# Kernel tuning notes

Measured on AMD Instinct MI355X. Metric: run time of the kernel, lower is better.

Reference implementation:

```python
import jax, jax.numpy as jnp
import numpy as np

N = 50000      # nodes
DEG = 32       # avg degree
E = N * DEG + N  # edges incl. self loops
IN_DIM = 512
H = 4          # heads
D = 128        # hidden per head
SLOPE = 0.2


def setup_inputs() -> dict:
    key = jax.random.key(0)
    ks = jax.random.split(key, 12)
    features = jax.random.normal(ks[0], (N, IN_DIM), dtype=jnp.float32)
    src_r = jax.random.randint(ks[1], (N * DEG,), 0, N)
    dst_r = jax.random.randint(ks[2], (N * DEG,), 0, N)
    loop = jnp.arange(N)
    src = jnp.concatenate([src_r, loop]).astype(jnp.int32)
    dst = jnp.concatenate([dst_r, loop]).astype(jnp.int32)
    ids = jax.random.randint(ks[3], (16,), 0, N)
    s0 = 1.0 / np.sqrt(IN_DIM)
    s1 = 1.0 / np.sqrt(H * D)
    fc_w0 = jax.random.normal(ks[4], (IN_DIM, H * D), dtype=jnp.float32) * s0
    attn_l0 = jax.random.normal(ks[5], (H, D), dtype=jnp.float32) * s1
    attn_r0 = jax.random.normal(ks[6], (H, D), dtype=jnp.float32) * s1
    bias0 = jnp.zeros((H * D,), dtype=jnp.float32)
    fc_w1 = jax.random.normal(ks[7], (H * D, H * D), dtype=jnp.float32) * s1
    attn_l1 = jax.random.normal(ks[8], (H, D), dtype=jnp.float32) * s1
    attn_r1 = jax.random.normal(ks[9], (H, D), dtype=jnp.float32) * s1
    bias1 = jnp.zeros((H * D,), dtype=jnp.float32)
    return dict(features=features, fc_w0=fc_w0, attn_l0=attn_l0, attn_r0=attn_r0,
                bias0=bias0, fc_w1=fc_w1, attn_l1=attn_l1, attn_r1=attn_r1,
                bias1=bias1, src=src, dst=dst, ids=ids)


def gat_layer(h, fc_w, attn_l, attn_r, bias, src, dst, residual):
    ft = (h @ fc_w).reshape(N, H, D)                     # [N,H,D]
    el = jnp.sum(ft * attn_l, axis=-1)                   # [N,H]
    er = jnp.sum(ft * attn_r, axis=-1)                   # [N,H]
    e = jax.nn.leaky_relu(el[src] + er[dst], SLOPE)      # [E,H]
    # edge softmax over incoming edges of each dst node (self-loops guarantee coverage)
    emax = jax.ops.segment_max(e, dst, num_segments=N)   # [N,H]
    ee = jnp.exp(e - emax[dst])
    esum = jax.ops.segment_sum(ee, dst, num_segments=N)  # [N,H]
    alpha = ee / esum[dst]                               # [E,H]
    out = jax.ops.segment_sum(alpha[:, :, None] * ft[src], dst, num_segments=N)  # [N,H,D]
    if residual:
        out = out + h.reshape(N, H, D)                   # res_fc is Identity (in == H*D)
    out = out + bias.reshape(1, H, D)
    out = jax.nn.elu(out)
    return out.reshape(N, H * D)


def reference(features, fc_w0, attn_l0, attn_r0, bias0, fc_w1, attn_l1, attn_r1,
              bias1, src, dst, ids):
    h = gat_layer(features, fc_w0, attn_l0, attn_r0, bias0, src, dst, residual=False)
    h = gat_layer(h, fc_w1, attn_l1, attn_r1, bias1, src, dst, residual=True)
    h = jnp.tanh(h)
    return h[ids]  # [B, H*D] gather per id2node lookup
```

## Files before the change

### kernel.cpp

```cpp
#include <hip/hip_runtime.h>
#include <hip/hip_bf16.h>

typedef short bf16x8 __attribute__((ext_vector_type(8)));
typedef float f32x4 __attribute__((ext_vector_type(4)));

#define HD 512
#define KDIM 512
#define NHEAD 4
#define DHEAD 128
#define C1CAP 1024
#define C2CAP 16384
#define E1CAP 2048
#define E2CAP 32768

struct PassSM {
    unsigned bm[1568];
    int2 eBuf[256];
    int fBuf[256];
    int sid[16];
    int eCnt, fCnt, eBase, fBase, s_c;
};

union PrepSM {
    PassSM pass;
    float tile[64][65];
    int s_c;
};

struct GemmSM {
    __hip_bfloat16 As[128][40];
    __hip_bfloat16 Bs[128][40];
    float pel[2][128];
    float perr[2][128];
};

__device__ int detect_bf16(const unsigned short* f, int* s_c) {
    int c = 0;
#pragma unroll
    for (int k = 0; k < 4; ++k) {
        unsigned short u = f[2 * (threadIdx.x + k * 256)];
        int e = (u >> 7) & 0xFF;
        c += (e >= 96 && e <= 140) ? 1 : 0;
    }
#pragma unroll
    for (int off = 32; off; off >>= 1) c += __shfl_xor(c, off, 64);
    if (threadIdx.x == 0) *s_c = 0;
    __syncthreads();
    if ((threadIdx.x & 63) == 0) atomicAdd(s_c, c);
    __syncthreads();
    int r = (*s_c > 512) ? 1 : 0;
    __syncthreads();
    return r;
}

template<int MODE>
__device__ void pass_scan(int pid, const int* __restrict__ src,
                          const int* __restrict__ dst, int E, int B,
                          const int* __restrict__ map1g, PassSM& sm,
                          int2* __restrict__ elist, int* ecnt, int ecap,
                          int* __restrict__ cntArr,
                          int* __restrict__ mapm, int* __restrict__ Flist,
                          int* nFr, int fcap) {
    const int t = threadIdx.x;
    const int nq = E >> 2;
    const int gid = pid * 256 + t;
    if (gid < nq) {
        const int4 d4 = ((const int4*)dst)[gid];
        const int dv[4] = {d4.x, d4.y, d4.z, d4.w};
#pragma unroll
        for (int k = 0; k < 4; ++k) {
            const int d = dv[k];
            if ((sm.bm[d >> 5] >> (d & 31)) & 1u) {
                const int e = 4 * gid + k;
                int slot;
                if (MODE == 0) {
                    slot = 0;
                    for (int q = 0; q < B; ++q) if (sm.sid[q] == d) slot = q;
                } else {
                    slot = map1g[d]; if (slot < 0) slot = 0;
                }
                int p = atomicAdd(&cntArr[slot], 1);
                int2 v; v.x = src[e]; v.y = slot | (p << (MODE == 0 ? 4 : 10));
                int pp = atomicAdd(&sm.eCnt, 1);
                if (pp < 256) sm.eBuf[pp] = v;
                else { int q = atomicAdd(ecnt, 1); if (q < ecap) elist[q] = v; }
                const int s = v.x;
                if (atomicCAS(&mapm[s], -1, -2) == -1) {
                    int q = atomicAdd(&sm.fCnt, 1);
                    if (q < 256) sm.fBuf[q] = s;
                    else {
                        int g2 = atomicAdd(nFr, 1);
                        if (g2 < fcap) { Flist[g2] = s; mapm[s] = g2; }
                        else mapm[s] = 0;
                    }
                }
            }
        }
    }
    __syncthreads();
    const int ne = (sm.eCnt < 256) ? sm.eCnt : 256;
    const int nf = (sm.fCnt < 256) ? sm.fCnt : 256;
    if (t == 0 && ne) sm.eBase = atomicAdd(ecnt, ne);
    if (t == 64 && nf) sm.fBase = atomicAdd(nFr, nf);
    __syncthreads();
    for (int i = t; i < ne; i += 256) {
        int pos = sm.eBase + i;
        if (pos < ecap) elist[pos] = sm.eBuf[i];
    }
    for (int i = t; i < nf; i += 256) {
        int q = sm.fBase + i; int s = sm.fBuf[i];
        if (q < fcap) { Flist[q] = s; mapm[s] = q; }
        else mapm[s] = 0;
    }
}

__device__ void gemm_tile(const __hip_bfloat16* __restrict__ A,
                          const __hip_bfloat16* __restrict__ Bt,
                          __hip_bfloat16* __restrict__ C,
                          const float* __restrict__ al_, const float* __restrict__ ar_,
                          float* __restrict__ el, float* __restrict__ er,
                          int cntv, int m0, int n0, GemmSM& sm) {
    const int t = threadIdx.x;
    const int lane = t & 63, wave = t >> 6;
    const int wm = (wave >> 1) * 64, wn = (wave & 1) * 64;
    const int fr = lane & 15, fk = (lane >> 4) * 8;
    const int r0 = t >> 2;
    const int c0 = (t & 3) * 8;

    int arow[2];
#pragma unroll
    for (int r = 0; r < 2; ++r) {
        int rr = m0 + r * 64 + r0;
        if (rr >= cntv) rr = cntv - 1;
        arow[r] = rr;
    }

    auto loadAB = [&](int kt, uint4 va[2], uint4 vb[2]) {
#pragma unroll
        for (int r = 0; r < 2; ++r) {
            va[r] = *(const uint4*)&A[(size_t)arow[r] * KDIM + kt + c0];
            int row = r * 64 + r0;
            vb[r] = *(const uint4*)&Bt[(size_t)(n0 + row) * KDIM + kt + c0];
        }
    };

    f32x4 acc[4][4];
#pragma unroll
    for (int i = 0; i < 4; ++i)
#pragma unroll
        for (int j = 0; j < 4; ++j)
#pragma unroll
            for (int r = 0; r < 4; ++r) acc[i][j][r] = 0.f;

    uint4 cva[2], cvb[2], nva[2], nvb[2];
    loadAB(0, cva, cvb);
    for (int kt = 0; kt < KDIM; kt += 32) {
#pragma unroll
        for (int r = 0; r < 2; ++r) {
            int row = r * 64 + r0;
            *(uint4*)&sm.As[row][c0] = cva[r];
            *(uint4*)&sm.Bs[row][c0] = cvb[r];
        }
        __syncthreads();
        if (kt + 32 < KDIM) loadAB(kt + 32, nva, nvb);
        bf16x8 af[4], bfr[4];
#pragma unroll
        for (int i = 0; i < 4; ++i) af[i]  = *(const bf16x8*)&sm.As[wm + i * 16 + fr][fk];
#pragma unroll
        for (int j = 0; j < 4; ++j) bfr[j] = *(const bf16x8*)&sm.Bs[wn + j * 16 + fr][fk];
#pragma unroll
        for (int i = 0; i < 4; ++i)
#pragma unroll
            for (int j = 0; j < 4; ++j)
                acc[i][j] = __builtin_amdgcn_mfma_f32_16x16x32_bf16(af[i], bfr[j], acc[i][j], 0, 0, 0);
        __syncthreads();
#pragma unroll
        for (int r = 0; r < 2; ++r) { cva[r] = nva[r]; cvb[r] = nvb[r]; }
    }

    const int cr = (lane >> 4) * 4;
    const int cc = lane & 15;
#pragma unroll
    for (int i = 0; i < 4; ++i)
#pragma unroll
        for (int j = 0; j < 4; ++j)
#pragma unroll
            for (int rg = 0; rg < 4; ++rg) {
                int m = m0 + wm + i * 16 + cr + rg;
                int n = n0 + wn + j * 16 + cc;
                C[(size_t)m * HD + n] = __float2bfloat16(acc[i][j][rg]);
            }

    const int h = n0 >> 7;
    float alv[4], arv[4];
#pragma unroll
    for (int j = 0; j < 4; ++j) {
        alv[j] = al_[h * DHEAD + wn + j * 16 + cc];
        arv[j] = ar_[h * DHEAD + wn + j * 16 + cc];
    }
#pragma unroll
    for (int i = 0; i < 4; ++i)
#pragma unroll
        for (int rg = 0; rg < 4; ++rg) {
            float sl = 0.f, sr = 0.f;
#pragma unroll
            for (int j = 0; j < 4; ++j) {
                float c = acc[i][j][rg];
                sl += c * alv[j];
                sr += c * arv[j];
            }
#pragma unroll
            for (int off = 1; off < 16; off <<= 1) {
                sl += __shfl_xor(sl, off, 16);
                sr += __shfl_xor(sr, off, 16);
            }
            if (cc == 0) {
                int row = wm + i * 16 + cr + rg;
                sm.pel[wn >> 6][row] = sl;
                sm.perr[wn >> 6][row] = sr;
            }
        }
    __syncthreads();
    if (t < 128) {
        int m = m0 + t;
        if (m < cntv) {
            el[m * NHEAD + h] = sm.pel[0][t] + sm.pel[1][t];
            er[m * NHEAD + h] = sm.perr[0][t] + sm.perr[1][t];
        }
    }
    __syncthreads();
}

__global__ __launch_bounds__(256) void prep_pass1_k(
    const void* __restrict__ features,
    const void* __restrict__ W0, const void* __restrict__ W1,
    __hip_bfloat16* __restrict__ Wt0, __hip_bfloat16* __restrict__ Wt1,
    const void* p0, const void* p1, const void* p2,
    const void* p3, const void* p4, const void* p5,
    float* __restrict__ smallc,
    const int* __restrict__ ids, int B, int* __restrict__ mapId,
    const int* __restrict__ src, const int* __restrict__ dst, int E,
    int2* __restrict__ E1l, int* __restrict__ counters,
    int* __restrict__ cnt1, int* __restrict__ map1, int* __restrict__ F1list) {
    __shared__ PrepSM sm;
    const int b = blockIdx.x;
    const int t = threadIdx.x;
    if (b < 128) {
        const int isbf = detect_bf16((const unsigned short*)features, &sm.s_c);
        const int mtx = b >> 6;
        const int tidx = b & 63;
        const int i0 = (tidx >> 3) * 64, j0 = (tidx & 7) * 64;
        const void* W = mtx ? W1 : W0;
        __hip_bfloat16* Wt = mtx ? Wt1 : Wt0;
        const int rr = t >> 6, cc = t & 63;
#pragma unroll
        for (int it = 0; it < 16; ++it) {
            int ii = rr + it * 4;
            size_t idx = (size_t)(i0 + ii) * 512 + j0 + cc;
            float v = isbf ? __bfloat162float(((const __hip_bfloat16*)W)[idx])
                           : ((const float*)W)[idx];
            sm.tile[ii][cc] = v;
        }
        __syncthreads();
#pragma unroll
        for (int it = 0; it < 16; ++it) {
            int jj = rr + it * 4;
            Wt[(size_t)(j0 + jj) * 512 + i0 + cc] = __float2bfloat16(sm.tile[cc][jj]);
        }
    } else if (b < 134) {
        const int isbf = detect_bf16((const unsigned short*)features, &sm.s_c);
        int which = b - 128;
        const void* p;
        switch (which) {
            case 0: p = p0; break;
            case 1: p = p1; break;
            case 2: p = p2; break;
            case 3: p = p3; break;
            case 4: p = p4; break;
            default: p = p5; break;
        }
#pragma unroll
        for (int r = 0; r < 2; ++r) {
            int e = t + r * 256;
            float v = isbf ? __bfloat162float(((const __hip_bfloat16*)p)[e])
                           : ((const float*)p)[e];
            smallc[which * 512 + e] = v;
        }
    } else if (b == 134) {
        if (t < B) atomicMax(&mapId[ids[t]], t);
    } else {
        const int pid = b - 135;
        for (int i = t; i < 1568; i += 256) sm.pass.bm[i] = 0u;
        if (t < 16) sm.pass.sid[t] = (t < B) ? ids[t] : -1;
        if (t == 0) { sm.pass.eCnt = 0; sm.pass.fCnt = 0; }
        __syncthreads();
        if (t < B) { int n = sm.pass.sid[t]; atomicOr(&sm.pass.bm[n >> 5], 1u << (n & 31)); }
        __syncthreads();
        pass_scan<0>(pid, src, dst, E, B, nullptr, sm.pass,
                     E1l, counters + 0, E1CAP, cnt1,
                     map1, F1list, counters + 2, C1CAP);
    }
}

__global__ __launch_bounds__(256) void pass2_k(
    const int* __restrict__ src, const int* __restrict__ dst, int E,
    const int* __restrict__ F1list, int* __restrict__ counters,
    const int* __restrict__ map1,
    int2* __restrict__ E2l, int* __restrict__ cnt2,
    int* __restrict__ map2, int* __restrict__ F2list) {
    __shared__ PassSM sm;
    const int t = threadIdx.x;
    for (int i = t; i < 1568; i += 256) sm.bm[i] = 0u;
    if (t == 0) { sm.eCnt = 0; sm.fCnt = 0; }
    __syncthreads();
    int nf1 = counters[2]; if (nf1 > C1CAP) nf1 = C1CAP;
    for (int i = t; i < nf1; i += 256) {
        int n = F1list[i];
        atomicOr(&sm.bm[n >> 5], 1u << (n & 31));
    }
    __syncthreads();
    pass_scan<1>(blockIdx.x, src, dst, E, 0, map1, sm,
                 E2l, counters + 1, E2CAP, cnt2,
                 map2, F2list, counters + 3, C2CAP);
}

__global__ __launch_bounds__(256) void gather_k(
    const void* __restrict__ feat, const int* __restrict__ F2list,
    const int* __restrict__ nF2p, __hip_bfloat16* __restrict__ Ac) {
    __shared__ int s_c;
    const int isbf = detect_bf16((const unsigned short*)feat, &s_c);
    int cnt = *nF2p; if (cnt > C2CAP) cnt = C2CAP;
    const int t = threadIdx.x;
    for (int b = blockIdx.x; b < cnt; b += gridDim.x) {
        int row = F2list[b];
        __hip_bfloat162 v;
        if (isbf) {
            v = *(const __hip_bfloat162*)&((const __hip_bfloat16*)feat)[(size_t)row * KDIM + t * 2];
        } else {
            const float2 f = *(const float2*)&((const float*)feat)[(size_t)row * KDIM + t * 2];
            v.x = __float2bfloat16(f.x);
            v.y = __float2bfloat16(f.y);
        }
        *(__hip_bfloat162*)&Ac[(size_t)b * KDIM + t * 2] = v;
    }
}

__global__ __launch_bounds__(256) void gemmel_k(
    int do_scatter,
    const int2* __restrict__ E1l, const int2* __restrict__ E2l,
    const int* __restrict__ counters,
    const int* __restrict__ cnt1, const int* __restrict__ cnt2,
    const int* __restrict__ map1, const int* __restrict__ map2,
    int* __restrict__ off1, int* __restrict__ off2,
    int* __restrict__ b1, int* __restrict__ b2,
    const __hip_bfloat16* __restrict__ A,
    const __hip_bfloat16* __restrict__ Bt, __hip_bfloat16* __restrict__ C,
    const float* __restrict__ al_, const float* __restrict__ ar_,
    float* __restrict__ el, float* __restrict__ er,
    const int* __restrict__ countp, int cap) {
    __shared__ alignas(16) GemmSM sm;
    const int t = threadIdx.x;
    const int bid = blockIdx.x;
    if (do_scatter && bid == 0) {
        int* soff = (int*)&sm;
        int* sc   = soff + 1024;
        int* s1   = sc + 256;
        int c0 = cnt2[t * 4 + 0], c1 = cnt2[t * 4 + 1];
        int c2 = cnt2[t * 4 + 2], c3 = cnt2[t * 4 + 3];
        int tsum = c0 + c1 + c2 + c3;
        sc[t] = tsum;
        __syncthreads();
        for (int off = 1; off < 256; off <<= 1) {
            int x = (t >= off) ? sc[t - off] : 0;
            __syncthreads();
            sc[t] += x;
            __syncthreads();
        }
        int run = sc[t] - tsum;
        int b4 = t * 4;
        off2[b4 + 0] = run; soff[b4 + 0] = run; run += c0;
        off2[b4 + 1] = run; soff[b4 + 1] = run; run += c1;
        off2[b4 + 2] = run; soff[b4 + 2] = run; run += c2;
        off2[b4 + 3] = run; soff[b4 + 3] = run; run += c3;
        if (t == 255) off2[1024] = run;
        if (t == 0) {
            int acc = 0;
            for (int i = 0; i < 16; ++i) { off1[i] = acc; s1[i] = acc; acc += cnt1[i]; }
            off1[16] = acc;
        }
        __syncthreads();
        int n2 = counters[1]; if (n2 > E2CAP) n2 = E2CAP;
        for (int i = t; i < n2; i += 256) {
            int2 v = E2l[i];
            int y = v.y & 1023, p = v.y >> 10;
            int pos = soff[y] + p;
            int r = map2[v.x]; if (r < 0) r = 0;
            if (pos < E2CAP) b2[pos] = r;
        }
        int n1 = counters[0]; if (n1 > E1CAP) n1 = E1CAP;
        for (int i = t; i < n1; i += 256) {
            int2 v = E1l[i];
            int y = v.y & 15, p = v.y >> 4;
            int pos = s1[y] + p;
            int r = map1[v.x]; if (r < 0) r = 0;
            if (pos < E1CAP) b1[pos] = r;
        }
        return;
    }
    const int nblk = (int)gridDim.x - (do_scatter ? 1 : 0);
    const int start = bid - (do_scatter ? 1 : 0);
    int cntv = *countp; if (cntv > cap) cntv = cap;
    const int nt = ((cntv + 127) >> 7) * 4;
    for (int tile = start; tile < nt; tile += nblk)
        gemm_tile(A, Bt, C, al_, ar_, el, er,
                  cntv, (tile >> 2) * 128, (tile & 3) * 128, sm);
}

__global__ __launch_bounds__(256) void agg1_k(
    const int* __restrict__ off2, const int* __restrict__ b2,
    const int* __restrict__ F1list, const int* __restrict__ map2,
    const int* __restrict__ nF1p,
    const float* __restrict__ el, const float* __restrict__ er,
    const __hip_bfloat16* __restrict__ ftc,
    const float* __restrict__ bias,
    __hip_bfloat16* __restrict__ outc) {
    int b = blockIdx.x;
    if (b >= *nF1p) return;
    int n = F1list[b];
    const int h = threadIdx.x >> 6, lane = threadIdx.x & 63;
    int rn = map2[n]; if (rn < 0) rn = 0;
    float ern = er[rn * NHEAD + h];
    int beg = off2[b], end = off2[b + 1];
    float m = -3.0e38f, l = 0.f, a0 = 0.f, a1 = 0.f;
    int i = beg;
    for (; i + 4 <= end; i += 4) {
        int r4[4]; float ev[4]; __hip_bfloat162 fv[4];
#pragma unroll
        for (int k = 0; k < 4; ++k) {
            int r = b2[i + k]; if ((unsigned)r >= C2CAP) r = 0;
            r4[k] = r;
        }
#pragma unroll
        for (int k = 0; k < 4; ++k) {
            ev[k] = el[r4[k] * NHEAD + h];
            fv[k] = *(const __hip_bfloat162*)&ftc[(size_t)r4[k] * HD + h * DHEAD + lane * 2];
        }
#pragma unroll
        for (int k = 0; k < 4; ++k) {
            float e = ev[k] + ern;
            e = (e >= 0.f) ? e : 0.2f * e;
            float mn = fmaxf(m, e);
            float sc = __expf(m - mn);
            float w  = __expf(e - mn);
            l  = l * sc + w;
            a0 = a0 * sc + w * __bfloat162float(fv[k].x);
            a1 = a1 * sc + w * __bfloat162float(fv[k].y);
            m = mn;
        }
    }
    for (; i < end; ++i) {
        int r2 = b2[i]; if ((unsigned)r2 >= C2CAP) r2 = 0;
        float e = el[r2 * NHEAD + h] + ern;
        e = (e >= 0.f) ? e : 0.2f * e;
        float mn = fmaxf(m, e);
        float sc = __expf(m - mn);
        float w  = __expf(e - mn);
        const __hip_bfloat162 f = *(const __hip_bfloat162*)&ftc[(size_t)r2 * HD + h * DHEAD + lane * 2];
        l  = l * sc + w;
        a0 = a0 * sc + w * __bfloat162float(f.x);
        a1 = a1 * sc + w * __bfloat162float(f.y);
        m = mn;
    }
    float inv = (l > 0.f) ? 1.0f / l : 0.f;
    float o0 = a0 * inv, o1 = a1 * inv;
    const float2 bb = *(const float2*)&bias[h * DHEAD + lane * 2];
    o0 += bb.x; o1 += bb.y;
    o0 = (o0 > 0.f) ? o0 : expm1f(o0);
    o1 = (o1 > 0.f) ? o1 : expm1f(o1);
    __hip_bfloat162 o2;
    o2.x = __float2bfloat16(o0);
    o2.y = __float2bfloat16(o1);
    *(__hip_bfloat162*)&outc[(size_t)b * HD + h * DHEAD + lane * 2] = o2;
}

__global__ __launch_bounds__(256) void agg2_k(
    const int* __restrict__ off1, const int* __restrict__ b1,
    const int* __restrict__ ids, const int* __restrict__ mapId,
    const int* __restrict__ map1,
    const float* __restrict__ el, const float* __restrict__ er,
    const __hip_bfloat16* __restrict__ ftc,
    const __hip_bfloat16* __restrict__ resc,
    const float* __restrict__ bias,
    void* __restrict__ out, const void* __restrict__ features) {
    __shared__ int s_c;
    const int isbf = detect_bf16((const unsigned short*)features, &s_c);
    int b = blockIdx.x;
    int n = ids[b];
    int slot = mapId[n]; if (slot < 0) slot = 0;
    const int h = threadIdx.x >> 6, lane = threadIdx.x & 63;
    int rn = map1[n]; if (rn < 0) rn = 0;
    float ern = er[rn * NHEAD + h];
    int beg = off1[slot], end = off1[slot + 1];
    float m = -3.0e38f, l = 0.f, a0 = 0.f, a1 = 0.f;
    int i = beg;
    for (; i + 4 <= end; i += 4) {
        int r4[4]; float ev[4]; __hip_bfloat162 fv[4];
#pragma unroll
        for (int k = 0; k < 4; ++k) {
            int r = b1[i + k]; if ((unsigned)r >= C1CAP) r = 0;
            r4[k] = r;
        }
#pragma unroll
        for (int k = 0; k < 4; ++k) {
            ev[k] = el[r4[k] * NHEAD + h];
            fv[k] = *(const __hip_bfloat162*)&ftc[(size_t)r4[k] * HD + h * DHEAD + lane * 2];
        }
#pragma unroll
        for (int k = 0; k < 4; ++k) {
            float e = ev[k] + ern;
            e = (e >= 0.f) ? e : 0.2f * e;
            float mn = fmaxf(m, e);
            float sc = __expf(m - mn);
            float w  = __expf(e - mn);
            l  = l * sc + w;
            a0 = a0 * sc + w * __bfloat162float(fv[k].x);
            a1 = a1 * sc + w * __bfloat162float(fv[k].y);
            m = mn;
        }
    }
    for (; i < end; ++i) {
        int r1 = b1[i]; if ((unsigned)r1 >= C1CAP) r1 = 0;
        float e = el[r1 * NHEAD + h] + ern;
        e = (e >= 0.f) ? e : 0.2f * e;
        float mn = fmaxf(m, e);
        float sc = __expf(m - mn);
        float w  = __expf(e - mn);
        const __hip_bfloat162 f = *(const __hip_bfloat162*)&ftc[(size_t)r1 * HD + h * DHEAD + lane * 2];
        l  = l * sc + w;
        a0 = a0 * sc + w * __bfloat162float(f.x);
        a1 = a1 * sc + w * __bfloat162float(f.y);
        m = mn;
    }
    float inv = (l > 0.f) ? 1.0f / l : 0.f;
    float o0 = a0 * inv, o1 = a1 * inv;
    const __hip_bfloat162 rv = *(const __hip_bfloat162*)&resc[(size_t)rn * HD + h * DHEAD + lane * 2];
    o0 += __bfloat162float(rv.x);
    o1 += __bfloat162float(rv.y);
    const float2 bb = *(const float2*)&bias[h * DHEAD + lane * 2];
    o0 += bb.x; o1 += bb.y;
    o0 = (o0 > 0.f) ? o0 : expm1f(o0);
    o1 = (o1 > 0.f) ? o1 : expm1f(o1);
    o0 = tanhf(o0);
    o1 = tanhf(o1);
    size_t oi = (size_t)b * HD + h * DHEAD + lane * 2;
    if (isbf) {
        __hip_bfloat162 o2;
        o2.x = __float2bfloat16(o0);
        o2.y = __float2bfloat16(o1);
        *(__hip_bfloat162*)&((__hip_bfloat16*)out)[oi] = o2;
    } else {
        float2 o2; o2.x = o0; o2.y = o1;
        *(float2*)&((float*)out)[oi] = o2;
    }
}

extern "C" void kernel_launch(void* const* d_in, const int* in_sizes, int n_in,
                              void* d_out, int out_size, void* d_ws, size_t ws_size,
                              hipStream_t stream) {
    const void* features = d_in[0];
    const int* src = (const int*)d_in[9];
    const int* dst = (const int*)d_in[10];
    const int* ids = (const int*)d_in[11];

    const int N = in_sizes[0] / KDIM;
    const int E = in_sizes[9];
    const int B = in_sizes[11];

    char* w = (char*)d_ws;
    auto alloc = [&](size_t bytes) {
        void* p = (void*)w;
        w += (bytes + 255) & ~(size_t)255;
        return p;
    };
    __hip_bfloat16* Wt0 = (__hip_bfloat16*)alloc(512 * 512 * 2);
    __hip_bfloat16* Wt1 = (__hip_bfloat16*)alloc(512 * 512 * 2);
    float* smallc = (float*)alloc(6 * 512 * 4);
    int* maps  = (int*)alloc((size_t)3 * N * 4);
    int* mapId = maps;
    int* map1  = maps + N;
    int* map2  = maps + 2 * N;
    int2* E1l  = (int2*)alloc((size_t)E1CAP * 8);
    int2* E2l  = (int2*)alloc((size_t)E2CAP * 8);
    int* F1list = (int*)alloc(C1CAP * 4);
    int* F2list = (int*)alloc(C2CAP * 4);
    const int zwords = 8 + 16 + 1024;
    int* zmem = (int*)alloc((size_t)zwords * 4);
    int* counters = zmem;
    int* cnt1 = zmem + 8;
    int* cnt2 = cnt1 + 16;
    int* off1 = (int*)alloc(17 * 4);
    int* off2 = (int*)alloc(1025 * 4);
    int* b1   = (int*)alloc(E1CAP * 4);
    int* b2   = (int*)alloc(E2CAP * 4);
    __hip_bfloat16* Ac   = (__hip_bfloat16*)alloc((size_t)C2CAP * KDIM * 2);
    __hip_bfloat16* ft0c = (__hip_bfloat16*)alloc((size_t)C2CAP * HD * 2);
    float* el0 = (float*)alloc((size_t)C2CAP * NHEAD * 4);
    float* er0 = (float*)alloc((size_t)C2CAP * NHEAD * 4);
    __hip_bfloat16* h1c  = (__hip_bfloat16*)alloc((size_t)C1CAP * HD * 2);
    __hip_bfloat16* ft1c = (__hip_bfloat16*)alloc((size_t)C1CAP * HD * 2);
    float* el1 = (float*)alloc((size_t)C1CAP * NHEAD * 4);
    float* er1 = (float*)alloc((size_t)C1CAP * NHEAD * 4);

    hipMemsetAsync(maps, 0xFF, (size_t)3 * N * 4, stream);
    hipMemsetAsync(zmem, 0, (size_t)zwords * 4, stream);

    float* al0c = smallc + 0 * 512;
    float* ar0c = smallc + 1 * 512;
    float* b0c  = smallc + 2 * 512;
    float* al1c = smallc + 3 * 512;
    float* ar1c = smallc + 4 * 512;
    float* b1c  = smallc + 5 * 512;

    const int nblk_scan = (E / 4 + 255) / 256;

    prep_pass1_k<<<135 + nblk_scan, 256, 0, stream>>>(
        features, d_in[1], d_in[5], Wt0, Wt1,
        d_in[2], d_in[3], d_in[4], d_in[6], d_in[7], d_in[8],
        smallc, ids, B, mapId, src, dst, E,
        E1l, counters, cnt1, map1, F1list);

    pass2_k<<<nblk_scan, 256, 0, stream>>>(src, dst, E, F1list, counters, map1,
                                           E2l, cnt2, map2, F2list);

    gather_k<<<2048, 256, 0, stream>>>(features, F2list, counters + 3, Ac);

    gemmel_k<<<513, 256, 0, stream>>>(1, E1l, E2l, counters, cnt1, cnt2,
                                      map1, map2, off1, off2, b1, b2,
                                      Ac, Wt0, ft0c, al0c, ar0c, el0, er0,
                                      counters + 3, C2CAP);

    agg1_k<<<C1CAP, 256, 0, stream>>>(off2, b2, F1list, map2, counters + 2,
                                      el0, er0, ft0c, b0c, h1c);

    gemmel_k<<<32, 256, 0, stream>>>(0, E1l, E2l, counters, cnt1, cnt2,
                                     map1, map2, off1, off2, b1, b2,
                                     h1c, Wt1, ft1c, al1c, ar1c, el1, er1,
                                     counters + 2, C1CAP);

    agg2_k<<<B, 256, 0, stream>>>(off1, b1, ids, mapId, map1,
                                  el1, er1, ft1c, h1c, b1c,
                                  d_out, features);
}
```

Baseline: 362.8 us.

## Move edge scatter into gather kernel and spread it across blocks

```diff
diff --git a/kernel.cpp b/kernel.cpp
--- a/kernel.cpp
+++ b/kernel.cpp
@@ -12,6 +12,7 @@
 #define C2CAP 16384
 #define E1CAP 2048
 #define E2CAP 32768
+#define SCATB 64
 
 struct PassSM {
     unsigned bm[1568];
@@ -324,47 +325,22 @@
                  map2, F2list, counters + 3, C2CAP);
 }
 
-__global__ __launch_bounds__(256) void gather_k(
+__global__ __launch_bounds__(256) void gathscat_k(
     const void* __restrict__ feat, const int* __restrict__ F2list,
-    const int* __restrict__ nF2p, __hip_bfloat16* __restrict__ Ac) {
-    __shared__ int s_c;
-    const int isbf = detect_bf16((const unsigned short*)feat, &s_c);
-    int cnt = *nF2p; if (cnt > C2CAP) cnt = C2CAP;
-    const int t = threadIdx.x;
-    for (int b = blockIdx.x; b < cnt; b += gridDim.x) {
-        int row = F2list[b];
-        __hip_bfloat162 v;
-        if (isbf) {
-            v = *(const __hip_bfloat162*)&((const __hip_bfloat16*)feat)[(size_t)row * KDIM + t * 2];
-        } else {
-            const float2 f = *(const float2*)&((const float*)feat)[(size_t)row * KDIM + t * 2];
-            v.x = __float2bfloat16(f.x);
-            v.y = __float2bfloat16(f.y);
-        }
-        *(__hip_bfloat162*)&Ac[(size_t)b * KDIM + t * 2] = v;
-    }
-}
-
-__global__ __launch_bounds__(256) void gemmel_k(
-    int do_scatter,
-    const int2* __restrict__ E1l, const int2* __restrict__ E2l,
     const int* __restrict__ counters,
     const int* __restrict__ cnt1, const int* __restrict__ cnt2,
+    const int2* __restrict__ E1l, const int2* __restrict__ E2l,
     const int* __restrict__ map1, const int* __restrict__ map2,
     int* __restrict__ off1, int* __restrict__ off2,
     int* __restrict__ b1, int* __restrict__ b2,
-    const __hip_bfloat16* __restrict__ A,
-    const __hip_bfloat16* __restrict__ Bt, __hip_bfloat16* __restrict__ C,
-    const float* __restrict__ al_, const float* __restrict__ ar_,
-    float* __restrict__ el, float* __restrict__ er,
-    const int* __restrict__ countp, int cap) {
-    __shared__ alignas(16) GemmSM sm;
+    __hip_bfloat16* __restrict__ Ac) {
+    __shared__ int soff[1024];
+    __shared__ int sc[256];
+    __shared__ int s1[16];
+    __shared__ int s_c;
     const int t = threadIdx.x;
-    const int bid = blockIdx.x;
-    if (do_scatter && bid == 0) {
-        int* soff = (int*)&sm;
-        int* sc   = soff + 1024;
-        int* s1   = sc + 256;
+    const int b = blockIdx.x;
+    if (b < SCATB) {
         int c0 = cnt2[t * 4 + 0], c1 = cnt2[t * 4 + 1];
         int c2 = cnt2[t * 4 + 2], c3 = cnt2[t * 4 + 3];
         int tsum = c0 + c1 + c2 + c3;
@@ -378,19 +354,27 @@
         }
         int run = sc[t] - tsum;
         int b4 = t * 4;
-        off2[b4 + 0] = run; soff[b4 + 0] = run; run += c0;
-        off2[b4 + 1] = run; soff[b4 + 1] = run; run += c1;
-        off2[b4 + 2] = run; soff[b4 + 2] = run; run += c2;
-        off2[b4 + 3] = run; soff[b4 + 3] = run; run += c3;
-        if (t == 255) off2[1024] = run;
+        soff[b4 + 0] = run; run += c0;
+        soff[b4 + 1] = run; run += c1;
+        soff[b4 + 2] = run; run += c2;
+        soff[b4 + 3] = run; run += c3;
         if (t == 0) {
             int acc = 0;
-            for (int i = 0; i < 16; ++i) { off1[i] = acc; s1[i] = acc; acc += cnt1[i]; }
-            off1[16] = acc;
+            for (int i = 0; i < 16; ++i) { s1[i] = acc; acc += cnt1[i]; }
+            if (b == 0) {
+                int a2 = 0;
+                for (int i = 0; i < 16; ++i) { off1[i] = a2; a2 += cnt1[i]; }
+                off1[16] = a2;
+            }
+        }
+        if (b == 0) {
+#pragma unroll
+            for (int k = 0; k < 4; ++k) off2[b4 + k] = soff[b4 + k];
+            if (t == 255) off2[1024] = run;
         }
         __syncthreads();
         int n2 = counters[1]; if (n2 > E2CAP) n2 = E2CAP;
-        for (int i = t; i < n2; i += 256) {
+        for (int i = b * 256 + t; i < n2; i += SCATB * 256) {
             int2 v = E2l[i];
             int y = v.y & 1023, p = v.y >> 10;
             int pos = soff[y] + p;
@@ -398,20 +382,41 @@
             if (pos < E2CAP) b2[pos] = r;
         }
         int n1 = counters[0]; if (n1 > E1CAP) n1 = E1CAP;
-        for (int i = t; i < n1; i += 256) {
+        for (int i = b * 256 + t; i < n1; i += SCATB * 256) {
             int2 v = E1l[i];
             int y = v.y & 15, p = v.y >> 4;
             int pos = s1[y] + p;
             int r = map1[v.x]; if (r < 0) r = 0;
             if (pos < E1CAP) b1[pos] = r;
         }
-        return;
-    }
-    const int nblk = (int)gridDim.x - (do_scatter ? 1 : 0);
-    const int start = bid - (do_scatter ? 1 : 0);
+    } else {
+        const int isbf = detect_bf16((const unsigned short*)feat, &s_c);
+        int cnt = counters[3]; if (cnt > C2CAP) cnt = C2CAP;
+        for (int bb = b - SCATB; bb < cnt; bb += (int)gridDim.x - SCATB) {
+            int row = F2list[bb];
+            __hip_bfloat162 v;
+            if (isbf) {
+                v = *(const __hip_bfloat162*)&((const __hip_bfloat16*)feat)[(size_t)row * KDIM + t * 2];
+            } else {
+                const float2 f = *(const float2*)&((const float*)feat)[(size_t)row * KDIM + t * 2];
+                v.x = __float2bfloat16(f.x);
+                v.y = __float2bfloat16(f.y);
+            }
+            *(__hip_bfloat162*)&Ac[(size_t)bb * KDIM + t * 2] = v;
+        }
+    }
+}
+
+__global__ __launch_bounds__(256) void gemmel_k(
+    const __hip_bfloat16* __restrict__ A,
+    const __hip_bfloat16* __restrict__ Bt, __hip_bfloat16* __restrict__ C,
+    const float* __restrict__ al_, const float* __restrict__ ar_,
+    float* __restrict__ el, float* __restrict__ er,
+    const int* __restrict__ countp, int cap) {
+    __shared__ alignas(16) GemmSM sm;
     int cntv = *countp; if (cntv > cap) cntv = cap;
     const int nt = ((cntv + 127) >> 7) * 4;
-    for (int tile = start; tile < nt; tile += nblk)
+    for (int tile = blockIdx.x; tile < nt; tile += (int)gridDim.x)
         gemm_tile(A, Bt, C, al_, ar_, el, er,
                   cntv, (tile >> 2) * 128, (tile & 3) * 128, sm);
 }
@@ -632,19 +637,17 @@
     pass2_k<<<nblk_scan, 256, 0, stream>>>(src, dst, E, F1list, counters, map1,
                                            E2l, cnt2, map2, F2list);
 
-    gather_k<<<2048, 256, 0, stream>>>(features, F2list, counters + 3, Ac);
-
-    gemmel_k<<<513, 256, 0, stream>>>(1, E1l, E2l, counters, cnt1, cnt2,
-                                      map1, map2, off1, off2, b1, b2,
-                                      Ac, Wt0, ft0c, al0c, ar0c, el0, er0,
+    gathscat_k<<<2048, 256, 0, stream>>>(features, F2list, counters, cnt1, cnt2,
+                                         E1l, E2l, map1, map2,
+                                         off1, off2, b1, b2, Ac);
+
+    gemmel_k<<<512, 256, 0, stream>>>(Ac, Wt0, ft0c, al0c, ar0c, el0, er0,
                                       counters + 3, C2CAP);
 
     agg1_k<<<C1CAP, 256, 0, stream>>>(off2, b2, F1list, map2, counters + 2,
                                       el0, er0, ft0c, b0c, h1c);
 
-    gemmel_k<<<32, 256, 0, stream>>>(0, E1l, E2l, counters, cnt1, cnt2,
-                                     map1, map2, off1, off2, b1, b2,
-                                     h1c, Wt1, ft1c, al1c, ar1c, el1, er1,
+    gemmel_k<<<32, 256, 0, stream>>>(h1c, Wt1, ft1c, al1c, ar1c, el1, er1,
                                      counters + 2, C1CAP);
 
     agg2_k<<<B, 256, 0, stream>>>(off1, b1, ids, mapId, map1,
```

Measured after the change: 332.8 us. -8.3%, faster.
